# Kernel tuning notes

Measured on AMD Instinct MI355X. Metric: run time of the kernel, lower is better.

## Reference

```python
import jax, jax.numpy as jnp
import numpy as np

B, N = 32, 512
TOKEN_DIM, FEAT_DIM = 256, 3133


def setup_inputs() -> dict:
    key = jax.random.key(0)
    ks = jax.random.split(key, 7)
    embeddings = jax.random.normal(ks[0], (B, N, 3072), dtype=jnp.float32)
    visibility_scores = jax.random.uniform(ks[1], (B, N, 6), dtype=jnp.float32)
    bbox_ltwh = jax.random.uniform(ks[2], (B, N, 4), dtype=jnp.float32)
    keypoints_xyc = jax.random.uniform(ks[3], (B, N, 17, 3), dtype=jnp.float32)
    feats_masks = jax.random.randint(ks[4], (B, N), 0, 2).astype(jnp.bool_)
    # nn.Linear(feat_dim, token_dim): W [out,in], b [out]
    bound = 1.0 / np.sqrt(FEAT_DIM)
    W = jax.random.uniform(ks[5], (TOKEN_DIM, FEAT_DIM), minval=-bound, maxval=bound, dtype=jnp.float32)
    b = jax.random.uniform(ks[6], (TOKEN_DIM,), minval=-bound, maxval=bound, dtype=jnp.float32)
    return {
        'embeddings': embeddings,
        'visibility_scores': visibility_scores,
        'bbox_ltwh': bbox_ltwh,
        'keypoints_xyc': keypoints_xyc,
        'feats_masks': feats_masks,
        'W': W,
        'b': b,
    }


def reference(embeddings, visibility_scores, bbox_ltwh, keypoints_xyc, feats_masks, W, b):
    Bm, Nm = feats_masks.shape
    kpts_flat = keypoints_xyc.reshape(Bm, Nm, -1)  # [B,N,51]
    cat_feats = jnp.concatenate([embeddings, visibility_scores, bbox_ltwh, kpts_flat], axis=-1)  # [B,N,3133]
    # gather -> linear -> scatter into zeros  ==  masked linear output
    y = jnp.einsum('bnf,tf->bnt', cat_feats, W) + b  # [B,N,token_dim]
    tokens = jnp.where(feats_masks[..., None], y, jnp.zeros((), dtype=y.dtype))
    return tokens
```

## Files before the change

kernel.cpp:

```cpp
#include <hip/hip_runtime.h>
#include <hip/hip_bf16.h>


#define TOKENS   16384
#define EMB      3072
#define KF       3133
#define KP       3136
#define TDIM     256
#define BKS      64
#define NSTEP    49
#define BM       64
#define BT       128
#define SP       72

typedef __attribute__((ext_vector_type(8))) short bf16x8;
typedef __attribute__((ext_vector_type(4))) float f32x4;

__device__ __forceinline__ unsigned int f2bf(float f) {
  __hip_bfloat16 h = __float2bfloat16(f);
  unsigned short u;
  __builtin_memcpy(&u, &h, 2);
  return (unsigned int)u;
}
__device__ __forceinline__ unsigned int pack2(float a, float b) {
  return f2bf(a) | (f2bf(b) << 16);
}

__global__ void pack_w_kernel(const float* __restrict__ W, unsigned short* __restrict__ wq) {
  int i = blockIdx.x * 256 + threadIdx.x;
  if (i >= TDIM * KP) return;
  int t = i / KP;
  int k = i - t * KP;
  float v = (k < KF) ? W[(size_t)t * KF + k] : 0.f;
  __hip_bfloat16 h = __float2bfloat16(v);
  unsigned short u; __builtin_memcpy(&u, &h, 2);
  wq[i] = u;
}

__global__ void pack_ext_kernel(const float* __restrict__ vis,
                                const float* __restrict__ bbox,
                                const float* __restrict__ kpt,
                                float* __restrict__ ext) {
  int i = blockIdx.x * 256 + threadIdx.x;
  int bn = i >> 6;
  int j  = i & 63;
  float v = 0.f;
  if (j < 6)       v = vis[bn * 6 + j];
  else if (j < 10) v = bbox[bn * 4 + (j - 6)];
  else if (j < 61) v = kpt[bn * 51 + (j - 10)];
  ext[i] = v;
}

__global__ __launch_bounds__(256, 2)
void linproj_kernel(const float* __restrict__ emb,
                    const int* __restrict__ mask,
                    const unsigned short* __restrict__ wq,
                    const float* __restrict__ ext,
                    const float* __restrict__ bias,
                    float* __restrict__ out) {
  __shared__ unsigned short lds[2 * BM * SP + 2 * BT * SP];

  const int tid = threadIdx.x;
  const int bid = blockIdx.x;
  const int mtile = ((bid >> 4) << 3) | (bid & 7);
  const int ttile = (bid >> 3) & 1;
  const int mBase = mtile * BM;
  const int tBase = ttile * BT;

  const int srow = tid >> 3;
  const int scol = (tid & 7) * 8;

  const int lane = tid & 63;
  const int wid  = tid >> 6;
  const int wm   = (wid >> 1) * 32;
  const int wt   = (wid & 1) * 64;
  const int lr   = lane & 15;
  const int lk   = lane >> 4;

  bool mk[2];
  const float* pA[2];
  const float* pE[2];
  const unsigned short* pW[4];
#pragma unroll
  for (int it = 0; it < 2; ++it) {
    int bn = mBase + srow + it * 32;
    mk[it] = (mask[bn] != 0);
    pA[it] = emb + (size_t)bn * EMB + scol;
    pE[it] = ext + (size_t)bn * BKS + scol;
  }
#pragma unroll
  for (int it = 0; it < 4; ++it) {
    int tg = tBase + srow + it * 32;
    pW[it] = wq + (size_t)tg * KP + scol;
  }

  f32x4 acc[2][4];
#pragma unroll
  for (int m = 0; m < 2; ++m)
#pragma unroll
    for (int t = 0; t < 4; ++t)
      acc[m][t] = (f32x4){0.f, 0.f, 0.f, 0.f};

  float4 fa[2][2];
  uint4  rwv[4];

  auto stage = [&](int s) {
#pragma unroll
    for (int it = 0; it < 2; ++it) {
      if (mk[it]) {
        const float* p = (s < NSTEP - 1) ? (pA[it] + s * BKS) : pE[it];
        fa[it][0] = *(const float4*)p;
        fa[it][1] = *(const float4*)(p + 4);
      } else {
        fa[it][0] = make_float4(0.f, 0.f, 0.f, 0.f);
        fa[it][1] = make_float4(0.f, 0.f, 0.f, 0.f);
      }
    }
#pragma unroll
    for (int it = 0; it < 4; ++it)
      rwv[it] = *(const uint4*)(pW[it] + s * BKS);
  };

  auto commit = [&](int b) {
    unsigned short* la = &lds[b * (BM * SP)];
    unsigned short* lw = &lds[2 * (BM * SP) + b * (BT * SP)];
#pragma unroll
    for (int it = 0; it < 2; ++it) {
      uint4 v;
      v.x = pack2(fa[it][0].x, fa[it][0].y);
      v.y = pack2(fa[it][0].z, fa[it][0].w);
      v.z = pack2(fa[it][1].x, fa[it][1].y);
      v.w = pack2(fa[it][1].z, fa[it][1].w);
      *(uint4*)&la[(srow + it * 32) * SP + scol] = v;
    }
#pragma unroll
    for (int it = 0; it < 4; ++it)
      *(uint4*)&lw[(srow + it * 32) * SP + scol] = rwv[it];
  };

  auto compute = [&](int b) {
    const unsigned short* la = &lds[b * (BM * SP)];
    const unsigned short* lw = &lds[2 * (BM * SP) + b * (BT * SP)];
#pragma unroll
    for (int kk = 0; kk < 2; ++kk) {
      const int col = kk * 32 + lk * 8;
      bf16x8 a0 = *(const bf16x8*)&la[(wm + lr) * SP + col];
      bf16x8 a1 = *(const bf16x8*)&la[(wm + 16 + lr) * SP + col];
#pragma unroll
      for (int t = 0; t < 4; ++t) {
        bf16x8 bv = *(const bf16x8*)&lw[(wt + t * 16 + lr) * SP + col];
        acc[0][t] = __builtin_amdgcn_mfma_f32_16x16x32_bf16(a0, bv, acc[0][t], 0, 0, 0);
        acc[1][t] = __builtin_amdgcn_mfma_f32_16x16x32_bf16(a1, bv, acc[1][t], 0, 0, 0);
      }
    }
  };

  stage(0);
  commit(0);
  __syncthreads();

  int cur = 0;
#pragma unroll 1
  for (int s = 0; s < NSTEP; ++s) {
    const bool more = (s + 1) < NSTEP;
    if (more) stage(s + 1);
    compute(cur);
    if (more) commit(cur ^ 1);
    __syncthreads();
    cur ^= 1;
  }

#pragma unroll
  for (int m = 0; m < 2; ++m) {
#pragma unroll
    for (int tf = 0; tf < 4; ++tf) {
      const int t = tBase + wt + tf * 16 + lr;
      const float bv = bias[t];
#pragma unroll
      for (int r = 0; r < 4; ++r) {
        const int bn = mBase + wm + m * 16 + lk * 4 + r;
        const float o = (mask[bn] != 0) ? (acc[m][tf][r] + bv) : 0.f;
        out[(size_t)bn * TDIM + t] = o;
      }
    }
  }
}

extern "C" void kernel_launch(void* const* d_in, const int* in_sizes, int n_in,
                              void* d_out, int out_size, void* d_ws, size_t ws_size,
                              hipStream_t stream) {
  const float* emb   = (const float*)d_in[0];
  const float* vis   = (const float*)d_in[1];
  const float* bbox  = (const float*)d_in[2];
  const float* kpt   = (const float*)d_in[3];
  const int*   mask  = (const int*)d_in[4];
  const float* W     = (const float*)d_in[5];
  const float* bias  = (const float*)d_in[6];
  float* out = (float*)d_out;

  float* ext          = (float*)d_ws;
  unsigned short* wq  = (unsigned short*)((char*)d_ws + (size_t)TOKENS * 64 * 4);

  pack_w_kernel  <<<(TDIM * KP + 255) / 256, 256, 0, stream>>>(W, wq);
  pack_ext_kernel<<<(TOKENS * 64) / 256,     256, 0, stream>>>(vis, bbox, kpt, ext);
  linproj_kernel <<<512, 256, 0, stream>>>(emb, mask, wq, ext, bias, out);
}
```

Before: 387.5 us.

## Load A directly into registers and stream pre-swizzled W tiles via global_load_lds

```diff
diff --git a/kernel.cpp b/kernel.cpp
--- a/kernel.cpp
+++ b/kernel.cpp
@@ -5,13 +5,11 @@
 #define TOKENS   16384
 #define EMB      3072
 #define KF       3133
-#define KP       3136
 #define TDIM     256
-#define BKS      64
 #define NSTEP    49
 #define BM       64
 #define BT       128
-#define SP       72
+#define WIMG     16384
 
 typedef __attribute__((ext_vector_type(8))) short bf16x8;
 typedef __attribute__((ext_vector_type(4))) float f32x4;
@@ -25,12 +23,34 @@
 __device__ __forceinline__ unsigned int pack2(float a, float b) {
   return f2bf(a) | (f2bf(b) << 16);
 }
+__device__ __forceinline__ bf16x8 cvt8(float4 a, float4 b) {
+  union { unsigned int u[4]; bf16x8 v; } r;
+  r.u[0] = pack2(a.x, a.y);
+  r.u[1] = pack2(a.z, a.w);
+  r.u[2] = pack2(b.x, b.y);
+  r.u[3] = pack2(b.z, b.w);
+  return r.v;
+}
+
+__device__ __forceinline__ void g2l16(const void* g, void* l) {
+  __builtin_amdgcn_global_load_lds(
+      (__attribute__((address_space(1))) void*)g,
+      (__attribute__((address_space(3))) void*)l,
+      16, 0, 0);
+}
 
 __global__ void pack_w_kernel(const float* __restrict__ W, unsigned short* __restrict__ wq) {
   int i = blockIdx.x * 256 + threadIdx.x;
-  if (i >= TDIM * KP) return;
-  int t = i / KP;
-  int k = i - t * KP;
+  if (i >= 2 * NSTEP * 8192) return;
+  int tt  = i / (NSTEP * 8192);
+  int r   = i % (NSTEP * 8192);
+  int s   = r >> 13;
+  int e   = r & 8191;
+  int row = e >> 6;
+  int cs  = e & 63;
+  int c   = cs ^ ((row & 7) << 3);
+  int k   = s * 64 + c;
+  int t   = tt * BT + row;
   float v = (k < KF) ? W[(size_t)t * KF + k] : 0.f;
   __hip_bfloat16 h = __float2bfloat16(v);
   unsigned short u; __builtin_memcpy(&u, &h, 2);
@@ -54,11 +74,11 @@
 __global__ __launch_bounds__(256, 2)
 void linproj_kernel(const float* __restrict__ emb,
                     const int* __restrict__ mask,
-                    const unsigned short* __restrict__ wq,
+                    const unsigned short* __restrict__ wqp,
                     const float* __restrict__ ext,
                     const float* __restrict__ bias,
                     float* __restrict__ out) {
-  __shared__ unsigned short lds[2 * BM * SP + 2 * BT * SP];
+  __shared__ unsigned short ldsW[2 * 8192];
 
   const int tid = threadIdx.x;
   const int bid = blockIdx.x;
@@ -67,9 +87,6 @@
   const int mBase = mtile * BM;
   const int tBase = ttile * BT;
 
-  const int srow = tid >> 3;
-  const int scol = (tid & 7) * 8;
-
   const int lane = tid & 63;
   const int wid  = tid >> 6;
   const int wm   = (wid >> 1) * 32;
@@ -77,22 +94,23 @@
   const int lr   = lane & 15;
   const int lk   = lane >> 4;
 
-  bool mk[2];
-  const float* pA[2];
-  const float* pE[2];
-  const unsigned short* pW[4];
-#pragma unroll
-  for (int it = 0; it < 2; ++it) {
-    int bn = mBase + srow + it * 32;
-    mk[it] = (mask[bn] != 0);
-    pA[it] = emb + (size_t)bn * EMB + scol;
-    pE[it] = ext + (size_t)bn * BKS + scol;
-  }
-#pragma unroll
-  for (int it = 0; it < 4; ++it) {
-    int tg = tBase + srow + it * 32;
-    pW[it] = wq + (size_t)tg * KP + scol;
-  }
+  const int row0 = mBase + wm + lr;
+  const int row1 = row0 + 16;
+  const bool m0 = (mask[row0] != 0);
+  const bool m1 = (mask[row1] != 0);
+  const int aoff = lk * 8;
+  const float* pA0 = emb + (size_t)row0 * EMB + aoff;
+  const float* pA1 = emb + (size_t)row1 * EMB + aoff;
+  const float* pE0 = ext + (size_t)row0 * 64 + aoff;
+  const float* pE1 = ext + (size_t)row1 * 64 + aoff;
+
+  const char* wsrc = (const char*)wqp + (size_t)ttile * (NSTEP * WIMG)
+                   + wid * 1024 + lane * 16;
+  char* lbase = (char*)ldsW;
+
+  const int swz0 = (lk * 16) ^ ((lr & 7) << 4);
+  const int swz1 = (64 + lk * 16) ^ ((lr & 7) << 4);
+  const int rbase = (wt + lr) * 128;
 
   f32x4 acc[2][4];
 #pragma unroll
@@ -101,86 +119,88 @@
     for (int t = 0; t < 4; ++t)
       acc[m][t] = (f32x4){0.f, 0.f, 0.f, 0.f};
 
-  float4 fa[2][2];
-  uint4  rwv[4];
-
-  auto stage = [&](int s) {
-#pragma unroll
-    for (int it = 0; it < 2; ++it) {
-      if (mk[it]) {
-        const float* p = (s < NSTEP - 1) ? (pA[it] + s * BKS) : pE[it];
-        fa[it][0] = *(const float4*)p;
-        fa[it][1] = *(const float4*)(p + 4);
-      } else {
-        fa[it][0] = make_float4(0.f, 0.f, 0.f, 0.f);
-        fa[it][1] = make_float4(0.f, 0.f, 0.f, 0.f);
-      }
-    }
-#pragma unroll
-    for (int it = 0; it < 4; ++it)
-      rwv[it] = *(const uint4*)(pW[it] + s * BKS);
+  float4 Aa[2][2][2], Ab[2][2][2];
+
+  auto stageW = [&](int s, int buf) {
+    const char* g = wsrc + (size_t)s * WIMG;
+    char* l = lbase + buf * WIMG + wid * 1024;
+#pragma unroll
+    for (int j = 0; j < 4; ++j)
+      g2l16(g + j * 4096, l + j * 4096);
   };
 
-  auto commit = [&](int b) {
-    unsigned short* la = &lds[b * (BM * SP)];
-    unsigned short* lw = &lds[2 * (BM * SP) + b * (BT * SP)];
-#pragma unroll
-    for (int it = 0; it < 2; ++it) {
-      uint4 v;
-      v.x = pack2(fa[it][0].x, fa[it][0].y);
-      v.y = pack2(fa[it][0].z, fa[it][0].w);
-      v.z = pack2(fa[it][1].x, fa[it][1].y);
-      v.w = pack2(fa[it][1].z, fa[it][1].w);
-      *(uint4*)&la[(srow + it * 32) * SP + scol] = v;
-    }
-#pragma unroll
-    for (int it = 0; it < 4; ++it)
-      *(uint4*)&lw[(srow + it * 32) * SP + scol] = rwv[it];
+  auto loadA = [&](int s, float4 (&A)[2][2][2]) {
+    const float* p0;
+    const float* p1;
+    if (s < NSTEP - 1) { p0 = pA0 + s * 64; p1 = pA1 + s * 64; }
+    else               { p0 = pE0;          p1 = pE1; }
+    if (m0) {
+#pragma unroll
+      for (int kk = 0; kk < 2; ++kk) {
+        A[0][kk][0] = *(const float4*)(p0 + kk * 32);
+        A[0][kk][1] = *(const float4*)(p0 + kk * 32 + 4);
+      }
+    } else {
+#pragma unroll
+      for (int kk = 0; kk < 2; ++kk)
+        A[0][kk][0] = A[0][kk][1] = make_float4(0.f, 0.f, 0.f, 0.f);
+    }
+    if (m1) {
+#pragma unroll
+      for (int kk = 0; kk < 2; ++kk) {
+        A[1][kk][0] = *(const float4*)(p1 + kk * 32);
+        A[1][kk][1] = *(const float4*)(p1 + kk * 32 + 4);
+      }
+    } else {
+#pragma unroll
+      for (int kk = 0; kk < 2; ++kk)
+        A[1][kk][0] = A[1][kk][1] = make_float4(0.f, 0.f, 0.f, 0.f);
+    }
   };
 
-  auto compute = [&](int b) {
-    const unsigned short* la = &lds[b * (BM * SP)];
-    const unsigned short* lw = &lds[2 * (BM * SP) + b * (BT * SP)];
+  auto compute = [&](int buf, const float4 (&A)[2][2][2]) {
+    const char* l = lbase + buf * WIMG;
 #pragma unroll
     for (int kk = 0; kk < 2; ++kk) {
-      const int col = kk * 32 + lk * 8;
-      bf16x8 a0 = *(const bf16x8*)&la[(wm + lr) * SP + col];
-      bf16x8 a1 = *(const bf16x8*)&la[(wm + 16 + lr) * SP + col];
-#pragma unroll
-      for (int t = 0; t < 4; ++t) {
-        bf16x8 bv = *(const bf16x8*)&lw[(wt + t * 16 + lr) * SP + col];
-        acc[0][t] = __builtin_amdgcn_mfma_f32_16x16x32_bf16(a0, bv, acc[0][t], 0, 0, 0);
-        acc[1][t] = __builtin_amdgcn_mfma_f32_16x16x32_bf16(a1, bv, acc[1][t], 0, 0, 0);
+      bf16x8 a0 = cvt8(A[0][kk][0], A[0][kk][1]);
+      bf16x8 a1 = cvt8(A[1][kk][0], A[1][kk][1]);
+      const int sw = kk ? swz1 : swz0;
+#pragma unroll
+      for (int tf = 0; tf < 4; ++tf) {
+        bf16x8 bv = *(const bf16x8*)(l + rbase + tf * 2048 + sw);
+        acc[0][tf] = __builtin_amdgcn_mfma_f32_16x16x32_bf16(a0, bv, acc[0][tf], 0, 0, 0);
+        acc[1][tf] = __builtin_amdgcn_mfma_f32_16x16x32_bf16(a1, bv, acc[1][tf], 0, 0, 0);
       }
     }
   };
 
-  stage(0);
-  commit(0);
+  stageW(0, 0);
+  loadA(0, Aa);
   __syncthreads();
 
-  int cur = 0;
 #pragma unroll 1
-  for (int s = 0; s < NSTEP; ++s) {
-    const bool more = (s + 1) < NSTEP;
-    if (more) stage(s + 1);
-    compute(cur);
-    if (more) commit(cur ^ 1);
+  for (int s = 0; s < NSTEP - 1; s += 2) {
+    stageW(s + 1, 1);
+    loadA(s + 1, Ab);
+    compute(0, Aa);
     __syncthreads();
-    cur ^= 1;
+    stageW(s + 2, 0);
+    loadA(s + 2, Aa);
+    compute(1, Ab);
+    __syncthreads();
   }
-
-#pragma unroll
-  for (int m = 0; m < 2; ++m) {
-#pragma unroll
-    for (int tf = 0; tf < 4; ++tf) {
-      const int t = tBase + wt + tf * 16 + lr;
-      const float bv = bias[t];
+  compute(0, Aa);
+
+#pragma unroll
+  for (int tf = 0; tf < 4; ++tf) {
+    const int t = tBase + wt + tf * 16 + lr;
+    const float bv = bias[t];
+#pragma unroll
+    for (int mf = 0; mf < 2; ++mf) {
 #pragma unroll
       for (int r = 0; r < 4; ++r) {
-        const int bn = mBase + wm + m * 16 + lk * 4 + r;
-        const float o = (mask[bn] != 0) ? (acc[m][tf][r] + bv) : 0.f;
-        out[(size_t)bn * TDIM + t] = o;
+        const int bn = mBase + wm + mf * 16 + lk * 4 + r;
+        out[(size_t)bn * TDIM + t] = (mask[bn] != 0) ? (acc[mf][tf][r] + bv) : 0.f;
       }
     }
   }
@@ -201,7 +221,7 @@
   float* ext          = (float*)d_ws;
   unsigned short* wq  = (unsigned short*)((char*)d_ws + (size_t)TOKENS * 64 * 4);
 
-  pack_w_kernel  <<<(TDIM * KP + 255) / 256, 256, 0, stream>>>(W, wq);
-  pack_ext_kernel<<<(TOKENS * 64) / 256,     256, 0, stream>>>(vis, bbox, kpt, ext);
+  pack_w_kernel  <<<(2 * NSTEP * 8192 + 255) / 256, 256, 0, stream>>>(W, wq);
+  pack_ext_kernel<<<(TOKENS * 64) / 256,            256, 0, stream>>>(vis, bbox, kpt, ext);
   linproj_kernel <<<512, 256, 0, stream>>>(emb, mask, wq, ext, bias, out);
 }
```

Measured after the change: 321.8 us. 1.2x faster.
